# Optimization experiments

Measured on AMD Instinct MI355X. Metric: run time of the kernel, lower is better.

## Reference

```python
import jax, jax.numpy as jnp
import numpy as np

B, H, S, D = 2, 16, 4096, 128


def setup_inputs() -> dict:
    key = jax.random.key(0)
    kq, kk, kv = jax.random.split(key, 3)
    q = jax.random.normal(kq, (B, H, S, D), dtype=jnp.float32)
    k = jax.random.normal(kk, (B, H, S, D), dtype=jnp.float32)
    v = jax.random.normal(kv, (B, H, S, D), dtype=jnp.float32)
    return {"q": q, "k": k, "v": v}


def reference(q, k, v):
    # kv: [B,H,D,D] = k^T @ v (contract over sequence)
    kv = jnp.einsum("bhsd,bhse->bhde", k, v)
    # out: v + q @ kv  -> [B,H,S,D]
    return v + jnp.einsum("bhsd,bhde->bhse", q, kv)
```

## Files before the change

kernel.cpp:

```cpp
#include <hip/hip_runtime.h>
#include <hip/hip_bf16.h>

#define BHN 32
#define SEQ 4096
#define DIM 128
#define TROWS 64

typedef __bf16 bf16x8 __attribute__((ext_vector_type(8)));
typedef __bf16 bf16x4 __attribute__((ext_vector_type(4)));
typedef float  f32x4  __attribute__((ext_vector_type(4)));

__device__ __forceinline__ bf16x8 cvt8(const float* f) {
    bf16x8 r;
#pragma unroll
    for (int i = 0; i < 8; ++i) r[i] = (__bf16)f[i];
    return r;
}

template<int CH>
__global__ __launch_bounds__(512) void p1_kv(const float* __restrict__ kin,
                                             const float* __restrict__ vin,
                                             __bf16* __restrict__ ws1) {
    constexpr int SR = SEQ / CH;
    constexpr int NT = SR / TROWS;

    __shared__ __align__(16) __bf16 kt[2][DIM][TROWS];
    __shared__ __align__(16) __bf16 vt[2][DIM][TROWS];

    const int bh    = blockIdx.x / CH;
    const int chunk = blockIdx.x % CH;
    const int tid = threadIdx.x;

    const int dcol = tid & 31;
    const int sgrp = tid >> 5;
    const int d0 = dcol * 4;
    const int s0 = sgrp * 4;

    const int w = tid >> 6;
    const int l = tid & 63;
    const int g = l >> 4;
    const int c = l & 15;

    const float* kb = kin + (size_t)bh * SEQ * DIM + (size_t)chunk * SR * DIM;
    const float* vb = vin + (size_t)bh * SEQ * DIM + (size_t)chunk * SR * DIM;

    f32x4 acc[8];
#pragma unroll
    for (int nt = 0; nt < 8; ++nt) acc[nt] = (f32x4){0.f, 0.f, 0.f, 0.f};

    f32x4 kr[4], vr[4];
    {
        const size_t off = (size_t)s0 * DIM + d0;
#pragma unroll
        for (int j = 0; j < 4; ++j) {
            kr[j] = *(const f32x4*)(kb + off + j * DIM);
            vr[j] = *(const f32x4*)(vb + off + j * DIM);
        }
    }

#pragma unroll
    for (int t = 0; t < NT; ++t) {
        const int p = t & 1;

#pragma unroll
        for (int jd = 0; jd < 4; ++jd) {
            const int dd  = d0 + jd;
            const int key = (dd & 7) ^ ((dd >> 2) & 7);
            const int o   = (((sgrp >> 1) ^ key) * 8) + (sgrp & 1) * 4;
            bf16x4 pk, pv;
#pragma unroll
            for (int j = 0; j < 4; ++j) {
                pk[j] = (__bf16)kr[j][jd];
                pv[j] = (__bf16)vr[j][jd];
            }
            *(bf16x4*)&kt[p][dd][o] = pk;
            *(bf16x4*)&vt[p][dd][o] = pv;
        }

        __builtin_amdgcn_sched_barrier(0);
        if (t + 1 < NT) {
            const size_t off = ((size_t)((t + 1) * TROWS + s0)) * DIM + d0;
#pragma unroll
            for (int j = 0; j < 4; ++j) {
                kr[j] = *(const f32x4*)(kb + off + j * DIM);
                vr[j] = *(const f32x4*)(vb + off + j * DIM);
            }
        }
        __builtin_amdgcn_sched_barrier(0);

        asm volatile("s_waitcnt lgkmcnt(0)" ::: "memory");
        __builtin_amdgcn_s_barrier();

        const int e    = w * 16 + c;
        const int keyE = (e & 7) ^ ((e >> 2) & 7);
#pragma unroll
        for (int st = 0; st < 2; ++st) {
            bf16x8 af = *(const bf16x8*)&vt[p][e][((st * 4 + g) ^ keyE) * 8];
#pragma unroll
            for (int nt = 0; nt < 8; ++nt) {
                const int d    = nt * 16 + c;
                const int keyD = (d & 7) ^ ((d >> 2) & 7);
                bf16x8 bfr = *(const bf16x8*)&kt[p][d][((st * 4 + g) ^ keyD) * 8];
                acc[nt] = __builtin_amdgcn_mfma_f32_16x16x32_bf16(af, bfr, acc[nt], 0, 0, 0);
            }
        }
    }

    __bf16* outp = ws1 + ((size_t)chunk * BHN + bh) * (DIM * DIM);
#pragma unroll
    for (int nt = 0; nt < 8; ++nt) {
        bf16x4 pq;
#pragma unroll
        for (int r = 0; r < 4; ++r) pq[r] = (__bf16)acc[nt][r];
        *(bf16x4*)(outp + nt * 2048 + tid * 4) = pq;
    }
}

template<int CH>
__global__ __launch_bounds__(256) void p1_reduce(const __bf16* __restrict__ ws1,
                                                 __bf16* __restrict__ ws2) {
    const int t   = blockIdx.x * 256 + threadIdx.x;
    const int bh  = t >> 11;
    const int r11 = t & 2047;

    const __bf16* base = ws1 + (size_t)bh * (DIM * DIM) + r11 * 8;
    float s[8] = {0.f, 0.f, 0.f, 0.f, 0.f, 0.f, 0.f, 0.f};
#pragma unroll
    for (int ch = 0; ch < CH; ++ch) {
        bf16x8 a = *(const bf16x8*)(base + (size_t)ch * BHN * DIM * DIM);
#pragma unroll
        for (int i = 0; i < 8; ++i) s[i] += (float)a[i];
    }

    __bf16* dst = ws2 + (size_t)bh * (DIM * DIM);
#pragma unroll
    for (int i = 0; i < 8; ++i) {
        const int f  = r11 * 8 + i;
        const int nt = f >> 11;
        const int wv = (f >> 8) & 7;
        const int gg = (f >> 6) & 3;
        const int cc = (f >> 2) & 15;
        const int r  = f & 3;
        const int e  = wv * 16 + gg * 4 + r;
        const int d  = nt * 16 + cc;
        dst[e * DIM + (((d >> 3) ^ (e & 15)) * 8) + (d & 7)] = (__bf16)s[i];
    }
}

__global__ __launch_bounds__(512) void p2_qkv(const float* __restrict__ qin,
                                              const float* __restrict__ vin,
                                              const __bf16* __restrict__ ws2,
                                              float* __restrict__ outp) {
    __shared__ __align__(16) __bf16 kvs[DIM * DIM];

    const int bh = blockIdx.x & 31;
    const int rc = blockIdx.x >> 5;
    const int tid = threadIdx.x;

    {
        const uint4* src = (const uint4*)(ws2 + (size_t)bh * DIM * DIM);
        uint4* dst = (uint4*)kvs;
#pragma unroll
        for (int j = 0; j < 4; ++j) dst[tid + j * 512] = src[tid + j * 512];
    }
    __syncthreads();

    const int w = tid >> 6;
    const int l = tid & 63;
    const int g = l >> 4;
    const int c = l & 15;
    const int s = rc * 128 + w * 16 + c;

    const float* qrow = qin + (size_t)bh * SEQ * DIM + (size_t)s * DIM + g * 8;
    bf16x8 bq[4];
#pragma unroll
    for (int ks = 0; ks < 4; ++ks) {
        f32x4 x = *(const f32x4*)(qrow + ks * 32);
        f32x4 y = *(const f32x4*)(qrow + ks * 32 + 4);
        float tmp[8];
        tmp[0]=x[0]; tmp[1]=x[1]; tmp[2]=x[2]; tmp[3]=x[3];
        tmp[4]=y[0]; tmp[5]=y[1]; tmp[6]=y[2]; tmp[7]=y[3];
        bq[ks] = cvt8(tmp);
    }

    f32x4 acc[8];
#pragma unroll
    for (int et = 0; et < 8; ++et) acc[et] = (f32x4){0.f, 0.f, 0.f, 0.f};

#pragma unroll
    for (int ks = 0; ks < 4; ++ks) {
#pragma unroll
        for (int et = 0; et < 8; ++et) {
            const int e = et * 16 + c;
            const int slot = (ks * 4 + g) ^ c;
            bf16x8 a = *(const bf16x8*)&kvs[e * DIM + slot * 8];
            acc[et] = __builtin_amdgcn_mfma_f32_16x16x32_bf16(a, bq[ks], acc[et], 0, 0, 0);
        }
    }

    const float* vb = vin + (size_t)bh * SEQ * DIM;
    float* ob = outp + (size_t)bh * SEQ * DIM;
#pragma unroll
    for (int et = 0; et < 8; ++et) {
        const size_t idx = (size_t)s * DIM + et * 16 + g * 4;
        f32x4 vv = *(const f32x4*)(vb + idx);
        f32x4 o = acc[et] + vv;
        *(f32x4*)(ob + idx) = o;
    }
}

extern "C" void kernel_launch(void* const* d_in, const int* in_sizes, int n_in,
                              void* d_out, int out_size, void* d_ws, size_t ws_size,
                              hipStream_t stream) {
    const float* q = (const float*)d_in[0];
    const float* k = (const float*)d_in[1];
    const float* v = (const float*)d_in[2];
    float* out = (float*)d_out;

    __bf16* ws2 = (__bf16*)d_ws;
    __bf16* ws1 = (__bf16*)d_ws + (size_t)BHN * DIM * DIM;

    p1_kv<16><<<BHN * 16, 512, 0, stream>>>(k, v, ws1);
    p1_reduce<16><<<256, 256, 0, stream>>>(ws1, ws2);
    p2_qkv<<<BHN * (SEQ / 128), 512, 0, stream>>>(q, v, ws2, out);
}
```

Baseline: 68.97 us.

## Fuse split-K reduction into kv kernel via last-block atomic counter

Removes the separate reduction kernel. Each (b,h) group of chunk blocks increments an atomic counter, and the last block to finish sums the 16 partial bf16 kv tiles and writes the swizzled result. This saves one kernel launch and its dispatch gap. In exchange it adds a memset launch, and the tail reduction for each head runs on a single block, which may serialize work at the end.

```diff
diff --git a/kernel.cpp b/kernel.cpp
--- a/kernel.cpp
+++ b/kernel.cpp
@@ -5,6 +5,7 @@
 #define SEQ 4096
 #define DIM 128
 #define TROWS 64
+#define CH 16
 
 typedef __bf16 bf16x8 __attribute__((ext_vector_type(8)));
 typedef __bf16 bf16x4 __attribute__((ext_vector_type(4)));
@@ -17,10 +18,11 @@
     return r;
 }
 
-template<int CH>
 __global__ __launch_bounds__(512) void p1_kv(const float* __restrict__ kin,
                                              const float* __restrict__ vin,
-                                             __bf16* __restrict__ ws1) {
+                                             __bf16* __restrict__ ws1,
+                                             __bf16* __restrict__ ws2,
+                                             int* __restrict__ cnt) {
     constexpr int SR = SEQ / CH;
     constexpr int NT = SR / TROWS;
 
@@ -114,36 +116,44 @@
         for (int r = 0; r < 4; ++r) pq[r] = (__bf16)acc[nt][r];
         *(bf16x4*)(outp + nt * 2048 + tid * 4) = pq;
     }
-}
-
-template<int CH>
-__global__ __launch_bounds__(256) void p1_reduce(const __bf16* __restrict__ ws1,
-                                                 __bf16* __restrict__ ws2) {
-    const int t   = blockIdx.x * 256 + threadIdx.x;
-    const int bh  = t >> 11;
-    const int r11 = t & 2047;
-
-    const __bf16* base = ws1 + (size_t)bh * (DIM * DIM) + r11 * 8;
-    float s[8] = {0.f, 0.f, 0.f, 0.f, 0.f, 0.f, 0.f, 0.f};
-#pragma unroll
-    for (int ch = 0; ch < CH; ++ch) {
-        bf16x8 a = *(const bf16x8*)(base + (size_t)ch * BHN * DIM * DIM);
-#pragma unroll
-        for (int i = 0; i < 8; ++i) s[i] += (float)a[i];
-    }
-
-    __bf16* dst = ws2 + (size_t)bh * (DIM * DIM);
-#pragma unroll
-    for (int i = 0; i < 8; ++i) {
-        const int f  = r11 * 8 + i;
-        const int nt = f >> 11;
-        const int wv = (f >> 8) & 7;
-        const int gg = (f >> 6) & 3;
-        const int cc = (f >> 2) & 15;
-        const int r  = f & 3;
-        const int e  = wv * 16 + gg * 4 + r;
-        const int d  = nt * 16 + cc;
-        dst[e * DIM + (((d >> 3) ^ (e & 15)) * 8) + (d & 7)] = (__bf16)s[i];
+
+    __syncthreads();
+    __shared__ int sLast;
+    if (tid == 0) {
+        int prev = __hip_atomic_fetch_add(&cnt[bh], 1, __ATOMIC_ACQ_REL,
+                                          __HIP_MEMORY_SCOPE_AGENT);
+        sLast = (prev == CH - 1);
+    }
+    __syncthreads();
+    if (sLast) {
+        __builtin_amdgcn_fence(__ATOMIC_ACQUIRE, "agent");
+
+        const __bf16* hb = ws1 + (size_t)bh * (DIM * DIM);
+        __bf16* dst = ws2 + (size_t)bh * (DIM * DIM);
+#pragma unroll
+        for (int rep = 0; rep < 4; ++rep) {
+            const int r11 = rep * 512 + tid;
+            const __bf16* base = hb + r11 * 8;
+            float s[8] = {0.f, 0.f, 0.f, 0.f, 0.f, 0.f, 0.f, 0.f};
+#pragma unroll
+            for (int ch = 0; ch < CH; ++ch) {
+                bf16x8 a = *(const bf16x8*)(base + (size_t)ch * BHN * DIM * DIM);
+#pragma unroll
+                for (int i = 0; i < 8; ++i) s[i] += (float)a[i];
+            }
+#pragma unroll
+            for (int i = 0; i < 8; ++i) {
+                const int f  = r11 * 8 + i;
+                const int nt = f >> 11;
+                const int wv = (f >> 8) & 7;
+                const int gg = (f >> 6) & 3;
+                const int cc = (f >> 2) & 15;
+                const int r  = f & 3;
+                const int e  = wv * 16 + gg * 4 + r;
+                const int d  = nt * 16 + cc;
+                dst[e * DIM + (((d >> 3) ^ (e & 15)) * 8) + (d & 7)] = (__bf16)s[i];
+            }
+        }
     }
 }
 
@@ -217,10 +227,12 @@
     const float* v = (const float*)d_in[2];
     float* out = (float*)d_out;
 
+    const size_t slab = (size_t)BHN * DIM * DIM * sizeof(__bf16);
     __bf16* ws2 = (__bf16*)d_ws;
-    __bf16* ws1 = (__bf16*)d_ws + (size_t)BHN * DIM * DIM;
-
-    p1_kv<16><<<BHN * 16, 512, 0, stream>>>(k, v, ws1);
-    p1_reduce<16><<<256, 256, 0, stream>>>(ws1, ws2);
+    __bf16* ws1 = (__bf16*)((char*)d_ws + slab);
+    int*    cnt = (int*)((char*)d_ws + slab * (1 + CH));
+
+    hipMemsetAsync(cnt, 0, BHN * sizeof(int), stream);
+    p1_kv<<<BHN * CH, 512, 0, stream>>>(k, v, ws1, ws2, cnt);
     p2_qkv<<<BHN * (SEQ / 128), 512, 0, stream>>>(q, v, ws2, out);
 }
```

Result: slower. 107.9 us (+56.4%).
